# Kernel optimization log

Measured on AMD Instinct MI355X. Metric: run time of the kernel, lower is better.

The kernel has to match this reference:

```python
import jax, jax.numpy as jnp
import numpy as np

QMIN, QMAX = -128, 127  # signed int8 range


def setup_inputs() -> dict:
    key = jax.random.key(0)
    k_x, k_w, k_b = jax.random.split(key, 3)
    N, C_in, H, W = 32, 128, 56, 56
    C_out, kH, kW = 256, 3, 3
    # int8-valued tensors carried as int32 (jax-friendly); values in [-128, 127]
    x = jax.random.randint(k_x, (N, C_in, H, W), 0, 256, dtype=jnp.int32) - 128
    weight = jax.random.randint(k_w, (C_out, C_in, kH, kW), 0, 256, dtype=jnp.int32) - 128
    # int32 bias, already quantized with scale s_in * s_w
    bias = jax.random.randint(k_b, (C_out,), -(2 ** 14), 2 ** 14, dtype=jnp.int32)
    return {
        "x": x,
        "weight": weight,
        "bias": bias,
        "input_scale": jnp.float32(0.02),
        "weight_scale": jnp.float32(0.005),
        "output_scale": jnp.float32(0.05),
        "input_zero_point": jnp.int32(-5),
        "output_zero_point": jnp.int32(3),
    }


def reference(x, weight, bias, input_scale, weight_scale, output_scale,
              input_zero_point, output_zero_point):
    # Dequant-style integer conv: shift input by its zero point (weights are
    # symmetric, zero point 0), accumulate in fp32 (stands in for int32 acc).
    x_f = (x - input_zero_point).astype(jnp.float32)
    w_f = weight.astype(jnp.float32)
    acc = jax.lax.conv_general_dilated(
        x_f, w_f,
        window_strides=(1, 1),
        padding=((1, 1), (1, 1)),
        dimension_numbers=("NCHW", "OIHW", "NCHW"),
    )
    acc = acc + bias.astype(jnp.float32)[None, :, None, None]
    # Requantize: scale fusion + output zero point, round, clamp to int8.
    requant_scale = input_scale * weight_scale / output_scale
    y = acc * requant_scale + output_zero_point.astype(jnp.float32)
    y_q = jnp.clip(jnp.round(y), QMIN, QMAX).astype(jnp.int8)
    return y_q
```

## Files before the change

kernel.cpp:

```cpp
#include <hip/hip_runtime.h>
#include <stdint.h>


#define NB 32
#define CI 128
#define HH 56
#define WW 56
#define CO 256
#define SPA (HH * WW)
#define HP 58
#define WP 64
#define XP2_BYTES (NB * HP * WP * CI)
#define BP_BYTES (9 * 2 * 4 * CO * 16)
#define ABUF (4 * 8192)

typedef int v4i __attribute__((ext_vector_type(4)));

__global__ __launch_bounds__(256) void prep_kernel(
    const int* __restrict__ x, const int* __restrict__ wgt,
    const int* __restrict__ bias, const int* __restrict__ zpi,
    int8_t* __restrict__ xp2, int8_t* __restrict__ bp, int* __restrict__ BG)
{
    __shared__ int sm[1824];
    const int tid = threadIdx.x, bid = blockIdx.x;
    const int zp = *zpi;
    const int zp4 = (zp & 255) * 0x01010101;

    if (bid < HH * NB) {
        const int n = bid / HH, h = bid % HH;
        #pragma unroll
        for (int it = 0; it < 7; ++it) {
            int j = tid + it * 256;
            int ci = j / 14, w4 = j - ci * 14;
            const v4i v = *(const v4i*)(x + ((n * CI + ci) * HH + h) * WW + w4 * 4);
            sm[w4 * 130 + ci] = (v.x & 255) | ((v.y & 255) << 8) |
                                ((v.z & 255) << 16) | (v.w << 24);
        }
        __syncthreads();
        int* od = (int*)xp2 + (n * HP + h + 1) * (WP * CI / 4);
        #pragma unroll
        for (int it = 0; it < 8; ++it) {
            int j = tid + it * 256;
            int widx = j >> 5, ci4 = j & 31;
            int val = zp4;
            if (widx >= 1 && widx <= WW) {
                int w = widx - 1;
                int base = (w >> 2) * 130 + ci4 * 4;
                int sh = (w & 3) * 8;
                val = ((sm[base] >> sh) & 0xff) | (((sm[base+1] >> sh) & 0xff) << 8) |
                      (((sm[base+2] >> sh) & 0xff) << 16) | ((sm[base+3] >> sh) << 24);
            }
            od[j ^ ((widx & 7) << 2)] = val;
        }
    } else if (bid < HH * NB + 2 * NB) {
        const int z = bid - HH * NB;
        const int n = z >> 1, hidx = (z & 1) ? (HP - 1) : 0;
        int* od = (int*)xp2 + (n * HP + hidx) * (WP * CI / 4);
        #pragma unroll
        for (int it = 0; it < 8; ++it) od[tid + it * 256] = zp4;
    } else {
        const int co = bid - (HH * NB + 2 * NB);
        for (int j = tid; j < 1152; j += 256) sm[j] = wgt[co * 1152 + j];
        __syncthreads();
        for (int j = tid; j < 288; j += 256) {
            int j4 = j & 3, q = (j >> 2) & 3, c64 = (j >> 4) & 1, t = j >> 5;
            int ci = c64 * 64 + q * 16 + j4 * 4;
            int b0 = sm[(ci + 0) * 9 + t] & 255, b1 = sm[(ci + 1) * 9 + t] & 255;
            int b2 = sm[(ci + 2) * 9 + t] & 255, b3 = sm[(ci + 3) * 9 + t];
            ((int*)bp)[((t * 2 + c64) * 4 + q) * 1024 + co * 4 + j4] =
                b0 | (b1 << 8) | (b2 << 16) | (b3 << 24);
        }
        if (tid < 9) {
            int s = 0;
            for (int ci = 0; ci < CI; ++ci) s += sm[ci * 9 + tid];
            sm[1152 + tid] = s;
        }
        __syncthreads();
        if (tid == 0) {
            int s9 = 0;
            for (int t = 0; t < 9; ++t) s9 += sm[1152 + t];
            BG[co] = bias[co] - zp * s9;
        }
    }
}

__global__ __launch_bounds__(256, 2) void qconv_mfma(
    const int8_t* __restrict__ xp2, const int8_t* __restrict__ bp,
    const int* __restrict__ BG,
    const float* __restrict__ si, const float* __restrict__ sw,
    const float* __restrict__ so, const int* __restrict__ zpo,
    int* __restrict__ out)
{
    const int tid  = threadIdx.x, lane = tid & 63, wid = tid >> 6;
    const int quad = lane >> 4, lo16 = lane & 15;
    const int bid  = blockIdx.x;
    const int xcd  = bid & 7, i = bid >> 3;
    const int n    = xcd * 4 + (i & 3);
    const int cb   = (i >> 2) & 1;
    const int sA   = i >> 3;
    const int ntiles = (i < 32) ? 4 : 3;
    const int cw   = cb * 128 + wid * 32;

    __shared__ __attribute__((aligned(16))) int8_t Asm[2][ABUF];

    const int8_t* src0 = xp2 + (((size_t)n * HP + 2 * sA) << 13);
    #pragma unroll
    for (int k = 0; k < 8; ++k) {
        const int u = wid + 4 * k;
        __builtin_amdgcn_global_load_lds(
            (const __attribute__((address_space(1))) void*)(src0 + (u << 10) + lane * 16),
            (__attribute__((address_space(3))) void*)(&Asm[0][u << 10]), 16, 0, 0);
    }

    v4i breg[9][2][2];
    #pragma unroll
    for (int t = 0; t < 9; ++t)
        #pragma unroll
        for (int c = 0; c < 2; ++c)
            #pragma unroll
            for (int ct = 0; ct < 2; ++ct) {
                breg[t][c][ct] = *(const v4i*)(bp + (((t * 2 + c) * 4 + quad) << 12) +
                                               ((cw + ct * 16 + lo16) << 4));
                asm volatile("" : "+v"(breg[t][c][ct]));
            }

    int bgv[2];
    #pragma unroll
    for (int ct = 0; ct < 2; ++ct) bgv[ct] = BG[cw + ct * 16 + lo16];
    const float rs = (*si) * (*sw) / (*so);
    const float zo = (float)(*zpo);

    int boff[7], sw3[7];
    #pragma unroll
    for (int mt = 0; mt < 7; ++mt) {
        const int ml = mt * 16 + lo16;
        const int srow = ml / 56, scol = ml - srow * 56;
        boff[mt] = srow * 8192 + scol * 128 + quad * 16;
        int s0 = ((scol + 0) & 7) << 4, s1 = ((scol + 1) & 7) << 4,
            s2 = ((scol + 2) & 7) << 4;
        sw3[mt] = s0 | (s1 << 8) | (s2 << 16);
    }

    int* optr0 = out + ((size_t)n * CO + cw + lo16) * SPA + quad * 4;
    int* optr1 = optr0 + 16 * SPA;

    __syncthreads();

    #pragma unroll 1
    for (int j = 0; j < ntiles; ++j) {
        const int s = sA + 8 * j;
        const int8_t* curA = Asm[j & 1];

        if (j + 1 < ntiles) {
            const int8_t* srcn = xp2 + (((size_t)n * HP + 2 * (s + 8)) << 13);
            int8_t* dst = (int8_t*)Asm[(j & 1) ^ 1];
            #pragma unroll
            for (int k = 0; k < 8; ++k) {
                const int u = wid + 4 * k;
                __builtin_amdgcn_global_load_lds(
                    (const __attribute__((address_space(1))) void*)(srcn + (u << 10) + lane * 16),
                    (__attribute__((address_space(3))) void*)(dst + (u << 10)), 16, 0, 0);
            }
        }
        __builtin_amdgcn_sched_barrier(0);

        v4i acc[7][2];
        #pragma unroll
        for (int mt = 0; mt < 7; ++mt) {
            acc[mt][0] = (v4i){0, 0, 0, 0};
            acc[mt][1] = (v4i){0, 0, 0, 0};
        }

        __builtin_amdgcn_s_setprio(1);
        #pragma unroll
        for (int tp = 0; tp < 9; ++tp) {
            const int dr = tp / 3, dc = tp % 3;
            #pragma unroll
            for (int mt = 0; mt < 7; ++mt) {
                const int off  = boff[mt] + dr * 8192 + dc * 128;
                const int phys = off ^ ((sw3[mt] >> (8 * dc)) & 0x70);
                v4i a0 = *(const v4i*)(curA + phys);
                v4i a1 = *(const v4i*)(curA + (phys ^ 64));
                acc[mt][0] = __builtin_amdgcn_mfma_i32_16x16x64_i8(a0, breg[tp][0][0], acc[mt][0], 0, 0, 0);
                acc[mt][1] = __builtin_amdgcn_mfma_i32_16x16x64_i8(a0, breg[tp][0][1], acc[mt][1], 0, 0, 0);
                acc[mt][0] = __builtin_amdgcn_mfma_i32_16x16x64_i8(a1, breg[tp][1][0], acc[mt][0], 0, 0, 0);
                acc[mt][1] = __builtin_amdgcn_mfma_i32_16x16x64_i8(a1, breg[tp][1][1], acc[mt][1], 0, 0, 0);
            }
        }
        __builtin_amdgcn_s_setprio(0);

        const int m0 = s * 112;
        #pragma unroll
        for (int mt = 0; mt < 7; ++mt) {
            v4i v0, v1;
            #pragma unroll
            for (int i4 = 0; i4 < 4; ++i4) {
                float y0 = rintf((float)(acc[mt][0][i4] + bgv[0]) * rs + zo);
                float y1 = rintf((float)(acc[mt][1][i4] + bgv[1]) * rs + zo);
                v0[i4] = (int)fminf(fmaxf(y0, -128.f), 127.f);
                v1[i4] = (int)fminf(fmaxf(y1, -128.f), 127.f);
            }
            *(v4i*)(optr0 + m0 + mt * 16) = v0;
            *(v4i*)(optr1 + m0 + mt * 16) = v1;
        }

        if (j + 1 < ntiles) {
            __builtin_amdgcn_sched_barrier(0);
            asm volatile("s_waitcnt vmcnt(14)" ::: "memory");
            __builtin_amdgcn_s_barrier();
            __builtin_amdgcn_sched_barrier(0);
        }
    }
}

extern "C" void kernel_launch(void* const* d_in, const int* in_sizes, int n_in,
                              void* d_out, int out_size, void* d_ws, size_t ws_size,
                              hipStream_t stream) {
    const int*   x    = (const int*)d_in[0];
    const int*   wgt  = (const int*)d_in[1];
    const int*   bias = (const int*)d_in[2];
    const float* si   = (const float*)d_in[3];
    const float* sw   = (const float*)d_in[4];
    const float* so   = (const float*)d_in[5];
    const int*   zpi  = (const int*)d_in[6];
    const int*   zpo  = (const int*)d_in[7];
    int* out = (int*)d_out;

    int8_t* xp2 = (int8_t*)d_ws;
    int8_t* bp  = xp2 + XP2_BYTES;
    int*    bg  = (int*)(bp + BP_BYTES);

    prep_kernel<<<HH * NB + 2 * NB + CO, 256, 0, stream>>>(x, wgt, bias, zpi, xp2, bp, bg);
    qconv_mfma<<<512, 256, 0, stream>>>(xp2, bp, bg, si, sw, so, zpo, out);
}
```

Baseline: 224.9 us.

## Stream weight fragments per tile instead of keeping all taps resident in registers

The 36 weight fragments per wave are no longer loaded once into registers for the whole kernel. Each tile now reloads them from global memory with a two-tap-ahead prefetch inside the tap loop. The aim is to cut VGPR pressure, which may raise occupancy or leave the scheduler more room. In exchange every tile issues extra global loads. Because vmcnt waits complete in issue order, waiting on the later weight loads may also force the double-buffered A prefetch to finish early, reducing load/compute overlap.

Result: faster. 187.6 us (-16.6%).

```diff
diff --git a/kernel.cpp b/kernel.cpp
--- a/kernel.cpp
+++ b/kernel.cpp
@@ -112,18 +112,6 @@
             (__attribute__((address_space(3))) void*)(&Asm[0][u << 10]), 16, 0, 0);
     }
 
-    v4i breg[9][2][2];
-    #pragma unroll
-    for (int t = 0; t < 9; ++t)
-        #pragma unroll
-        for (int c = 0; c < 2; ++c)
-            #pragma unroll
-            for (int ct = 0; ct < 2; ++ct) {
-                breg[t][c][ct] = *(const v4i*)(bp + (((t * 2 + c) * 4 + quad) << 12) +
-                                               ((cw + ct * 16 + lo16) << 4));
-                asm volatile("" : "+v"(breg[t][c][ct]));
-            }
-
     int bgv[2];
     #pragma unroll
     for (int ct = 0; ct < 2; ++ct) bgv[ct] = BG[cw + ct * 16 + lo16];
@@ -141,15 +129,29 @@
         sw3[mt] = s0 | (s1 << 8) | (s2 << 16);
     }
 
+    const int8_t* bwav = bp + ((size_t)quad << 12) + ((cw + lo16) << 4);
+
     int* optr0 = out + ((size_t)n * CO + cw + lo16) * SPA + quad * 4;
     int* optr1 = optr0 + 16 * SPA;
 
     __syncthreads();
+
+    #define BLOAD(tp) {                                                        \
+        const int8_t* bb = bwav + ((tp) * 8 << 12);                            \
+        asm volatile("" : "+v"(bb));                                           \
+        bt[tp][0] = *(const v4i*)(bb);                                         \
+        bt[tp][1] = *(const v4i*)(bb + 256);                                   \
+        bt[tp][2] = *(const v4i*)(bb + 16384);                                 \
+        bt[tp][3] = *(const v4i*)(bb + 16384 + 256);                           \
+    }
 
     #pragma unroll 1
     for (int j = 0; j < ntiles; ++j) {
         const int s = sA + 8 * j;
         const int8_t* curA = Asm[j & 1];
+
+        v4i bt[9][4];
+        BLOAD(0); BLOAD(1);
 
         if (j + 1 < ntiles) {
             const int8_t* srcn = xp2 + (((size_t)n * HP + 2 * (s + 8)) << 13);
@@ -174,6 +176,7 @@
         __builtin_amdgcn_s_setprio(1);
         #pragma unroll
         for (int tp = 0; tp < 9; ++tp) {
+            if (tp + 2 <= 8) BLOAD(tp + 2);
             const int dr = tp / 3, dc = tp % 3;
             #pragma unroll
             for (int mt = 0; mt < 7; ++mt) {
@@ -181,10 +184,10 @@
                 const int phys = off ^ ((sw3[mt] >> (8 * dc)) & 0x70);
                 v4i a0 = *(const v4i*)(curA + phys);
                 v4i a1 = *(const v4i*)(curA + (phys ^ 64));
-                acc[mt][0] = __builtin_amdgcn_mfma_i32_16x16x64_i8(a0, breg[tp][0][0], acc[mt][0], 0, 0, 0);
-                acc[mt][1] = __builtin_amdgcn_mfma_i32_16x16x64_i8(a0, breg[tp][0][1], acc[mt][1], 0, 0, 0);
-                acc[mt][0] = __builtin_amdgcn_mfma_i32_16x16x64_i8(a1, breg[tp][1][0], acc[mt][0], 0, 0, 0);
-                acc[mt][1] = __builtin_amdgcn_mfma_i32_16x16x64_i8(a1, breg[tp][1][1], acc[mt][1], 0, 0, 0);
+                acc[mt][0] = __builtin_amdgcn_mfma_i32_16x16x64_i8(a0, bt[tp][0], acc[mt][0], 0, 0, 0);
+                acc[mt][1] = __builtin_amdgcn_mfma_i32_16x16x64_i8(a0, bt[tp][1], acc[mt][1], 0, 0, 0);
+                acc[mt][0] = __builtin_amdgcn_mfma_i32_16x16x64_i8(a1, bt[tp][2], acc[mt][0], 0, 0, 0);
+                acc[mt][1] = __builtin_amdgcn_mfma_i32_16x16x64_i8(a1, bt[tp][3], acc[mt][1], 0, 0, 0);
             }
         }
         __builtin_amdgcn_s_setprio(0);
@@ -211,6 +214,7 @@
             __builtin_amdgcn_sched_barrier(0);
         }
     }
+    #undef BLOAD
 }
 
 extern "C" void kernel_launch(void* const* d_in, const int* in_sizes, int n_in,
```
